# Kernel tuning notes

Measured on AMD Instinct MI355X. Metric: run time of the kernel, lower is better.

## Reference

```python
import jax, jax.numpy as jnp
import numpy as np

GRASPNESS_THRESHOLD = 0.001
M_POINT = 2048
NUM_VIEW = 800
NUM_ANGLE = 12
NUM_DEPTH = 7
B, N, C = 2, 20480, 256
ND, NS = 16384, 512


def generate_grasp_views(n=NUM_VIEW):
    # Fibonacci sphere sampling of unit approach vectors (graspnet convention)
    phi = (np.sqrt(5.0) - 1.0) / 2.0
    i = np.arange(n)
    zi = (2.0 * i + 1.0) / n - 1.0
    r = np.sqrt(np.maximum(1.0 - zi * zi, 0.0))
    xi = r * np.cos(2.0 * np.pi * i * phi)
    yi = r * np.sin(2.0 * np.pi * i * phi)
    return jnp.asarray(np.stack([xi, yi, zi], axis=1), dtype=jnp.float32)  # [n,3], unit norm


def masked_fps(xyz, mask, m):
    # furthest point sampling restricted to mask==True points; xyz [N,3]
    big = jnp.float32(1e10)
    d0 = jnp.where(mask, big, jnp.float32(-1.0))  # invalid never selected
    start = jnp.argmax(mask)  # first valid index (matches compact-then-FPS start at 0)

    def step(carry, _):
        dists, last = carry
        d = jnp.sum((xyz - xyz[last]) ** 2, axis=-1)
        dists = jnp.minimum(dists, jnp.where(mask, d, jnp.float32(-1.0)))
        return (dists, jnp.argmax(dists)), last

    _, idx = jax.lax.scan(step, (d0, start), None, length=m)
    return idx  # [m] int32


def setup_inputs() -> dict:
    key = jax.random.key(0)
    ks = jax.random.split(key, 9)
    return {
        "seed_xyz": jax.random.normal(ks[0], (B, N, 3), jnp.float32),
        "seed_features": jax.random.normal(ks[1], (B, N, C), jnp.float32),
        "graspness_score": jax.random.normal(ks[2], (B, N), jnp.float32),
        "dense_points": jax.random.normal(ks[3], (B, ND, 3), jnp.float32),
        "sparse_points": jax.random.normal(ks[4], (B, NS, 3), jnp.float32),
        "normalized_scores": jax.random.uniform(ks[5], (B, NS), jnp.float32),
        "approach_directions": jax.random.normal(ks[6], (B, NS, 3, 3), jnp.float32),
        "normalized_view_score": jax.random.uniform(ks[7], (B, NS, 3), jnp.float32),
        "normalized_grasp_score": jax.random.uniform(ks[8], (B, NS, 3, NUM_ANGLE, NUM_DEPTH), jnp.float32),
    }


def reference(seed_xyz, seed_features, graspness_score, dense_points, sparse_points,
              normalized_scores, approach_directions, normalized_view_score,
              normalized_grasp_score):
    # ---- stage 1: graspness mask -> masked FPS -> gather xyz/features ----
    graspable = graspness_score > GRASPNESS_THRESHOLD            # [B,N]
    fps_idx = jax.vmap(lambda x, m: masked_fps(x, m, M_POINT))(seed_xyz, graspable)  # [B,M]
    xyz_g = jnp.take_along_axis(seed_xyz, fps_idx[..., None], axis=1)       # [B,M,3]
    feat_g = jnp.take_along_axis(seed_features, fps_idx[..., None], axis=1)  # [B,M,C]

    # ---- stage 2: affordance label via 2-NN of dense points in sparse points ----
    valid = jnp.any(sparse_points != 0.0, axis=-1)               # [B,NS]
    d2 = (jnp.sum(dense_points ** 2, -1)[:, :, None]
          + jnp.sum(sparse_points ** 2, -1)[:, None, :]
          - 2.0 * jnp.einsum('bnd,bmd->bnm', dense_points, sparse_points))  # [B,ND,NS]
    d2 = jnp.where(valid[:, None, :], d2, jnp.float32(1e10))
    _, nn2 = jax.lax.top_k(-d2, 2)                               # [B,ND,2] two nearest
    nn_scores = jax.vmap(lambda s, i: s[i])(normalized_scores, nn2)
    affordance = jnp.mean(nn_scores, axis=-1)                    # [B,ND]

    # ---- stage 3: 1-NN view assignment against 800 template views + scatter ----
    views = generate_grasp_views(NUM_VIEW)                       # [V,3] unit vectors
    # argmin ||a - v||^2 over unit-norm v == argmax a.v
    view_inds = jnp.argmax(jnp.einsum('bnkd,vd->bnkv', approach_directions, views), axis=-1)  # [B,NS,3]
    b_idx = jnp.arange(B)[:, None, None]
    n_idx = jnp.arange(NS)[None, :, None]
    vm = valid.astype(jnp.float32)[:, :, None]                   # zero-out padded sparse rows
    view_scores = jnp.zeros((B, NS, NUM_VIEW), jnp.float32).at[
        b_idx, n_idx, view_inds].set(normalized_view_score * vm)  # [B,NS,V]
    grasp_scores = jnp.zeros((B, NS, NUM_VIEW, NUM_ANGLE, NUM_DEPTH), jnp.float32).at[
        b_idx, n_idx, view_inds].set(normalized_grasp_score * vm[..., None, None])  # [B,NS,V,12,7]
    return xyz_g, feat_g, affordance, view_scores, grasp_scores
```

## Files before the change

kernel.cpp:

```cpp
#include <hip/hip_runtime.h>
#include <math.h>

#define B_   2
#define N_   20480
#define C_   256
#define M_   2048
#define ND_  16384
#define NS_  512
#define NV_  800
#define NAD_ 84

#define OFF_XYZ  0LL
#define OFF_FEAT 12288LL
#define OFF_AFF  1060864LL
#define OFF_VS   1093632LL
#define OFF_GS   1912832LL
#define TOTAL_OUT 70725632LL

#define CAP_ 11264

#define FPS_T 512
#define FPS_P (CAP_ / FPS_T)
#define FPS_W (FPS_T / 64)
#define CPP_  (N_ / FPS_T)

#define NB_FPS 2
#define NB_AFF ((B_ * ND_) / FPS_T)
#define NB_SC  ((B_ * NS_) / FPS_W)
#define GRID_  (NB_FPS + NB_AFF + NB_SC)

union SMem {
    struct {
        float sx[CAP_], sy[CAP_], sz[CAP_];
        alignas(16) unsigned long long s_e[2][FPS_W];
        int s_slot[M_];
        int wsum[FPS_W];
    } fps;
    struct {
        float sx[NS_], sy[NS_], sz[NS_], ss2[NS_], ssc[NS_];
        unsigned char sval[NS_];
    } aff;
    struct { float vx[NV_], vy[NV_], vz[NV_]; } sc;
};

template <int CTRL>
__device__ __forceinline__ unsigned long long dpp_max_u64(unsigned long long k) {
    int olo = __builtin_amdgcn_update_dpp(0, (int)(unsigned)k, CTRL, 0xF, 0xF, true);
    int ohi = __builtin_amdgcn_update_dpp(0, (int)(unsigned)(k >> 32), CTRL, 0xF, 0xF, true);
    unsigned long long ok = ((unsigned long long)(unsigned)ohi << 32) | (unsigned)olo;
    return ok > k ? ok : k;
}

__device__ __forceinline__ unsigned long long wave_argmax_key(unsigned long long k) {
    k = dpp_max_u64<0xB1>(k);
    k = dpp_max_u64<0x4E>(k);
    k = dpp_max_u64<0x141>(k);
    k = dpp_max_u64<0x140>(k);
    k = dpp_max_u64<0x142>(k);
    k = dpp_max_u64<0x143>(k);
    return k;
}

__device__ __forceinline__ unsigned long long group8_max_u64(unsigned long long k) {
    k = dpp_max_u64<0xB1>(k);
    k = dpp_max_u64<0x4E>(k);
    k = dpp_max_u64<0x141>(k);
    return k;
}

__device__ void fps_role(SMem& sm, int b,
                         const float* __restrict__ xyz,
                         const float* __restrict__ gs,
                         int* __restrict__ ic_g, int* __restrict__ fps_idx)
{
    const float* __restrict__ X = xyz + (size_t)b * N_ * 3;
    const float* __restrict__ G = gs + (size_t)b * N_;
    int* __restrict__ IC = ic_g + (size_t)b * CAP_;
    const int t = threadIdx.x, lane = t & 63, wid = t >> 6;

    const int base = t * CPP_;
    int c = 0;
    for (int i = 0; i < CPP_; i++) c += (G[base + i] > 0.001f) ? 1 : 0;
    int inc = c;
#pragma unroll
    for (int o = 1; o < 64; o <<= 1) {
        int v = __shfl_up(inc, o);
        if (lane >= o) inc += v;
    }
    if (lane == 63) sm.fps.wsum[wid] = inc;
    __syncthreads();
    int off = inc - c;
    for (int w = 0; w < wid; w++) off += sm.fps.wsum[w];
    int total = 0;
#pragma unroll
    for (int w = 0; w < FPS_W; w++) total += sm.fps.wsum[w];

    for (int i = 0; i < CPP_; i++) {
        int p = base + i;
        if (G[p] > 0.001f && off < CAP_) {
            sm.fps.sx[off] = X[3 * p];
            sm.fps.sy[off] = X[3 * p + 1];
            sm.fps.sz[off] = X[3 * p + 2];
            IC[off] = p;
            off++;
        }
    }
    const int cv = (total > CAP_) ? CAP_ : total;
    for (int s = cv + t; s < CAP_; s += FPS_T) {
        sm.fps.sx[s] = 0.0f; sm.fps.sy[s] = 0.0f; sm.fps.sz[s] = 0.0f; IC[s] = 0;
    }
    if (t == 0) sm.fps.s_slot[0] = 0;
    __syncthreads();

    float px[FPS_P], py[FPS_P], pz[FPS_P], dd[FPS_P];
#pragma unroll
    for (int i = 0; i < FPS_P; i++) {
        int s = t + FPS_T * i;
        px[i] = sm.fps.sx[s];
        py[i] = sm.fps.sy[s];
        pz[i] = sm.fps.sz[s];
        dd[i] = (s < cv) ? 1e10f : -1.0f;
        asm volatile("" : "+v"(px[i]), "+v"(py[i]), "+v"(pz[i]));
    }
    const int cbase = (lane == 1) ? CAP_ : ((lane == 2) ? 2 * CAP_ : 0);

    float xl = sm.fps.sx[0], yl = sm.fps.sy[0], zl = sm.fps.sz[0];

    for (int it = 1; it < M_; it++) {
        float bv = -2.0f;
        int bli = 0;
#pragma unroll
        for (int i = 0; i < FPS_P; i++) {
            float dx = __fsub_rn(px[i], xl);
            float dy = __fsub_rn(py[i], yl);
            float dz = __fsub_rn(pz[i], zl);
            float d = __fadd_rn(__fadd_rn(__fmul_rn(dx, dx), __fmul_rn(dy, dy)),
                                __fmul_rn(dz, dz));
            float nd = fminf(dd[i], d);
            dd[i] = nd;
            if (nd > bv) { bv = nd; bli = i; }
        }
        unsigned vb = __float_as_uint(bv);
        unsigned mono = (vb & 0x80000000u) ? ~vb : (vb | 0x80000000u);
        int bi = t + FPS_T * bli;
        unsigned long long k = ((unsigned long long)mono << 32)
                             | (unsigned)(0x7FFFFFFF - bi);
        k = wave_argmax_key(k);
        const int par = it & 1;
        if (lane == 63) sm.fps.s_e[par][wid] = k;
        __syncthreads();
        unsigned long long e = sm.fps.s_e[par][lane & 7];
        e = group8_max_u64(e);
        int slot = 0x7FFFFFFF - (int)(unsigned)e;
        if (t == 0) sm.fps.s_slot[it] = slot;
        float cval = sm.fps.sx[cbase + slot];
        int cw = __float_as_int(cval);
        xl = __int_as_float(__builtin_amdgcn_readlane(cw, 0));
        yl = __int_as_float(__builtin_amdgcn_readlane(cw, 1));
        zl = __int_as_float(__builtin_amdgcn_readlane(cw, 2));
    }
    __syncthreads();
    for (int j = t; j < M_; j += FPS_T)
        fps_idx[b * M_ + j] = IC[sm.fps.s_slot[j]];
}

__device__ void aff_role(SMem& sm, int abid,
                         const float* __restrict__ dense,
                         const float* __restrict__ sparse,
                         const float* __restrict__ scores,
                         float* __restrict__ out)
{
    const int t = threadIdx.x;
    const int g = abid * FPS_T + t;
    const int b = g >> 14;
    const int n = g & (ND_ - 1);
    const float* SP = sparse + (size_t)b * NS_ * 3;
    for (int j = t; j < NS_; j += FPS_T) {
        float x = SP[3 * j], y = SP[3 * j + 1], z = SP[3 * j + 2];
        sm.aff.sx[j] = x; sm.aff.sy[j] = y; sm.aff.sz[j] = z;
        sm.aff.ss2[j] = __fadd_rn(__fadd_rn(__fmul_rn(x, x), __fmul_rn(y, y)),
                                  __fmul_rn(z, z));
        sm.aff.sval[j] = (x != 0.0f) || (y != 0.0f) || (z != 0.0f);
        sm.aff.ssc[j] = scores[(size_t)b * NS_ + j];
    }
    __syncthreads();
    const float* D = dense + ((size_t)b * ND_ + n) * 3;
    float x = D[0], y = D[1], z = D[2];
    float ds2 = __fadd_rn(__fadd_rn(__fmul_rn(x, x), __fmul_rn(y, y)),
                          __fmul_rn(z, z));
    float b1 = 1e30f, b2 = 1e30f;
    int i1 = 0, i2 = 0;
    for (int j = 0; j < NS_; j++) {
        float dot = __fadd_rn(__fadd_rn(__fmul_rn(x, sm.aff.sx[j]),
                                        __fmul_rn(y, sm.aff.sy[j])),
                              __fmul_rn(z, sm.aff.sz[j]));
        float d2 = __fsub_rn(__fadd_rn(ds2, sm.aff.ss2[j]), __fmul_rn(2.0f, dot));
        d2 = sm.aff.sval[j] ? d2 : 1e10f;
        if (d2 < b1)      { b2 = b1; i2 = i1; b1 = d2; i1 = j; }
        else if (d2 < b2) { b2 = d2; i2 = j; }
    }
    out[OFF_AFF + (size_t)b * ND_ + n] = (sm.aff.ssc[i1] + sm.aff.ssc[i2]) * 0.5f;
}

__device__ void scatter_role(SMem& sm, int sbid,
                             const float* __restrict__ sparse,
                             const float* __restrict__ appr,
                             const float* __restrict__ nvs,
                             const float* __restrict__ ngs,
                             float* __restrict__ out)
{
    const int t = threadIdx.x;
    for (int i = t; i < NV_; i += FPS_T) {
        const double phi = (sqrt(5.0) - 1.0) * 0.5;
        double zi = (2.0 * (double)i + 1.0) / (double)NV_ - 1.0;
        double r2 = 1.0 - zi * zi;
        if (r2 < 0.0) r2 = 0.0;
        double r = sqrt(r2);
        double ang = ((2.0 * 3.14159265358979311600) * (double)i) * phi;
        sm.sc.vx[i] = (float)(r * cos(ang));
        sm.sc.vy[i] = (float)(r * sin(ang));
        sm.sc.vz[i] = (float)zi;
    }
    const int r0 = sbid * FPS_W;
    {
        float4* vs4 = (float4*)(out + OFF_VS + (size_t)r0 * NV_);
        for (int i = t; i < (FPS_W * NV_) / 4; i += FPS_T)
            vs4[i] = make_float4(0.f, 0.f, 0.f, 0.f);
        float4* gs4 = (float4*)(out + OFF_GS + (size_t)r0 * NV_ * NAD_);
        for (int i = t; i < (FPS_W * NV_ * NAD_) / 4; i += FPS_T)
            gs4[i] = make_float4(0.f, 0.f, 0.f, 0.f);
    }
    __syncthreads();

    const int wid = t >> 6, lane = t & 63;
    const int gw = r0 + wid;
    const int b = gw / NS_, n = gw % NS_;
    const float* SP = sparse + ((size_t)b * NS_ + n) * 3;
    float vm = ((SP[0] != 0.0f) || (SP[1] != 0.0f) || (SP[2] != 0.0f)) ? 1.0f : 0.0f;

    int vind[3];
#pragma unroll
    for (int k = 0; k < 3; k++) {
        const float* A = appr + (((size_t)b * NS_ + n) * 3 + k) * 3;
        float ax = A[0], ay = A[1], az = A[2];
        float bv = -1e30f;
        int bi = 0x7fffffff;
        for (int v = lane; v < NV_; v += 64) {
            float d = __fadd_rn(__fadd_rn(__fmul_rn(ax, sm.sc.vx[v]),
                                          __fmul_rn(ay, sm.sc.vy[v])),
                                __fmul_rn(az, sm.sc.vz[v]));
            if (d > bv) { bv = d; bi = v; }
        }
#pragma unroll
        for (int o = 32; o > 0; o >>= 1) {
            float ov = __shfl_xor(bv, o);
            int   oi = __shfl_xor(bi, o);
            if (ov > bv || (ov == bv && oi < bi)) { bv = ov; bi = oi; }
        }
        vind[k] = bi;
    }
    bool wk0 = (vind[0] != vind[1]) && (vind[0] != vind[2]);
    bool wk1 = (vind[1] != vind[2]);
    bool wk[3] = { wk0, wk1, true };

    size_t row = (size_t)b * NS_ + n;
    if (lane < 3 && wk[lane]) {
        out[OFF_VS + row * NV_ + vind[lane]] = nvs[row * 3 + lane] * vm;
    }
#pragma unroll
    for (int k = 0; k < 3; k++) {
        if (!wk[k]) continue;
        const float* S = ngs + (row * 3 + k) * NAD_;
        float* Dst = out + OFF_GS + (row * NV_ + (size_t)vind[k]) * NAD_;
        for (int j = lane; j < NAD_; j += 64) Dst[j] = S[j] * vm;
    }
}

__global__ __launch_bounds__(FPS_T)
__attribute__((amdgpu_waves_per_eu(2, 2)))
void mega_kernel(
    const float* __restrict__ xyz, const float* __restrict__ gs,
    int* __restrict__ ic_g, int* __restrict__ fps_idx,
    const float* __restrict__ dense, const float* __restrict__ sparse,
    const float* __restrict__ scores, const float* __restrict__ appr,
    const float* __restrict__ nvs, const float* __restrict__ ngs,
    float* __restrict__ out)
{
    __shared__ SMem sm;
    const int bid = blockIdx.x;
    if (bid < NB_FPS) {
        fps_role(sm, bid, xyz, gs, ic_g, fps_idx);
    } else if (bid < NB_FPS + NB_AFF) {
        aff_role(sm, bid - NB_FPS, dense, sparse, scores, out);
    } else {
        scatter_role(sm, bid - NB_FPS - NB_AFF, sparse, appr, nvs, ngs, out);
    }
}

__global__ __launch_bounds__(256) void gather_kernel(
    const float* __restrict__ xyz, const float* __restrict__ feat,
    const int* __restrict__ fps_idx, float* __restrict__ out)
{
    int bm = blockIdx.x;
    int b = bm / M_;
    int idx = fps_idx[bm];
    const float* src = feat + ((size_t)b * N_ + idx) * C_;
    float* dst = out + OFF_FEAT + (size_t)bm * C_;
    dst[threadIdx.x] = src[threadIdx.x];
    if (threadIdx.x < 3)
        out[OFF_XYZ + (size_t)bm * 3 + threadIdx.x] =
            xyz[((size_t)b * N_ + idx) * 3 + threadIdx.x];
}

extern "C" void kernel_launch(void* const* d_in, const int* in_sizes, int n_in,
                              void* d_out, int out_size, void* d_ws, size_t ws_size,
                              hipStream_t stream) {
    const float* seed_xyz      = (const float*)d_in[0];
    const float* seed_features = (const float*)d_in[1];
    const float* graspness     = (const float*)d_in[2];
    const float* dense_points  = (const float*)d_in[3];
    const float* sparse_points = (const float*)d_in[4];
    const float* norm_scores   = (const float*)d_in[5];
    const float* approach      = (const float*)d_in[6];
    const float* nvs           = (const float*)d_in[7];
    const float* ngs           = (const float*)d_in[8];
    float* out = (float*)d_out;

    int* fps_idx = (int*)d_ws;
    int* ic      = (int*)((char*)d_ws + 16384);

    mega_kernel<<<dim3(GRID_), dim3(FPS_T), 0, stream>>>(
        seed_xyz, graspness, ic, fps_idx,
        dense_points, sparse_points, norm_scores,
        approach, nvs, ngs, out);
    gather_kernel<<<dim3(B_ * M_), dim3(256), 0, stream>>>(seed_xyz, seed_features,
                                                           fps_idx, out);
}
```

Before: 2.581 ms.

## Spatially sort FPS candidates into Morton cells and skip waves via bounding-box bounds

Valid points are bucketed into an 8x8x8 Morton-ordered grid with a histogram and scatter, so each thread's contiguous slots hold spatially clustered points. Each wave computes its bounding box, and on every FPS iteration skips the distance update when the lower bound from the new centroid to the box exceeds the wave's current max min-distance, reusing its cached key. Ties are broken by original index to keep the reference argmax order. CAP is reduced slightly. This adds atomics and extra setup passes and depends on exact tie and bound reasoning to stay correct.

```diff
diff --git a/kernel.cpp b/kernel.cpp
--- a/kernel.cpp
+++ b/kernel.cpp
@@ -17,7 +17,7 @@
 #define OFF_GS   1912832LL
 #define TOTAL_OUT 70725632LL
 
-#define CAP_ 11264
+#define CAP_ 10752
 
 #define FPS_T 512
 #define FPS_P (CAP_ / FPS_T)
@@ -35,6 +35,7 @@
         alignas(16) unsigned long long s_e[2][FPS_W];
         int s_slot[M_];
         int wsum[FPS_W];
+        int first_slot;
     } fps;
     struct {
         float sx[NS_], sy[NS_], sz[NS_], ss2[NS_], ssc[NS_];
@@ -50,7 +51,6 @@
     unsigned long long ok = ((unsigned long long)(unsigned)ohi << 32) | (unsigned)olo;
     return ok > k ? ok : k;
 }
-
 __device__ __forceinline__ unsigned long long wave_argmax_key(unsigned long long k) {
     k = dpp_max_u64<0xB1>(k);
     k = dpp_max_u64<0x4E>(k);
@@ -60,12 +60,19 @@
     k = dpp_max_u64<0x143>(k);
     return k;
 }
-
 __device__ __forceinline__ unsigned long long group8_max_u64(unsigned long long k) {
     k = dpp_max_u64<0xB1>(k);
     k = dpp_max_u64<0x4E>(k);
     k = dpp_max_u64<0x141>(k);
     return k;
+}
+
+__device__ __forceinline__ int q8(float v) {
+    int q = (int)floorf(v + 4.0f);
+    return q < 0 ? 0 : (q > 7 ? 7 : q);
+}
+__device__ __forceinline__ int spread3(int v) {
+    return (v & 1) | ((v & 2) << 2) | ((v & 4) << 4);
 }
 
 __device__ void fps_role(SMem& sm, int b,
@@ -77,10 +84,15 @@
     const float* __restrict__ G = gs + (size_t)b * N_;
     int* __restrict__ IC = ic_g + (size_t)b * CAP_;
     const int t = threadIdx.x, lane = t & 63, wid = t >> 6;
-
-    const int base = t * CPP_;
-    int c = 0;
-    for (int i = 0; i < CPP_; i++) c += (G[base + i] > 0.001f) ? 1 : 0;
+    int* hist   = sm.fps.s_slot;
+    int* cursor = sm.fps.s_slot + 512;
+
+    const int base_in = t * CPP_;
+    int c = 0, firstv = 0x7fffffff;
+    for (int i = 0; i < CPP_; i++) {
+        int p = base_in + i;
+        if (G[p] > 0.001f) { c++; if (p < firstv) firstv = p; }
+    }
     int inc = c;
 #pragma unroll
     for (int o = 1; o < 64; o <<= 1) {
@@ -88,70 +100,149 @@
         if (lane >= o) inc += v;
     }
     if (lane == 63) sm.fps.wsum[wid] = inc;
-    __syncthreads();
-    int off = inc - c;
-    for (int w = 0; w < wid; w++) off += sm.fps.wsum[w];
+    if (t == 0) sm.fps.first_slot = 0;
+    hist[t] = 0;
+    __syncthreads();
     int total = 0;
 #pragma unroll
     for (int w = 0; w < FPS_W; w++) total += sm.fps.wsum[w];
+    const int cv = (total > CAP_) ? CAP_ : total;
+    int fv = firstv;
+#pragma unroll
+    for (int o = 32; o > 0; o >>= 1) fv = min(fv, __shfl_xor(fv, o));
+    __syncthreads();
+    if (lane == 0) sm.fps.wsum[wid] = fv;
+    __syncthreads();
+#pragma unroll
+    for (int w = 0; w < FPS_W; w++) fv = min(fv, sm.fps.wsum[w]);
 
     for (int i = 0; i < CPP_; i++) {
-        int p = base + i;
-        if (G[p] > 0.001f && off < CAP_) {
-            sm.fps.sx[off] = X[3 * p];
-            sm.fps.sy[off] = X[3 * p + 1];
-            sm.fps.sz[off] = X[3 * p + 2];
-            IC[off] = p;
-            off++;
+        int p = base_in + i;
+        if (G[p] > 0.001f) {
+            int cell = (spread3(q8(X[3 * p])) << 2)
+                     | (spread3(q8(X[3 * p + 1])) << 1)
+                     | spread3(q8(X[3 * p + 2]));
+            atomicAdd(&hist[cell], 1);
         }
     }
-    const int cv = (total > CAP_) ? CAP_ : total;
+    __syncthreads();
+
+    int hv = hist[t];
+    int hinc = hv;
+#pragma unroll
+    for (int o = 1; o < 64; o <<= 1) {
+        int v = __shfl_up(hinc, o);
+        if (lane >= o) hinc += v;
+    }
+    __syncthreads();
+    if (lane == 63) sm.fps.wsum[wid] = hinc;
+    __syncthreads();
+    int hoff = hinc - hv;
+    for (int w = 0; w < wid; w++) hoff += sm.fps.wsum[w];
+    cursor[t] = hoff;
+    __syncthreads();
+
+    for (int i = 0; i < CPP_; i++) {
+        int p = base_in + i;
+        if (G[p] > 0.001f) {
+            float x = X[3 * p], y = X[3 * p + 1], z = X[3 * p + 2];
+            int cell = (spread3(q8(x)) << 2) | (spread3(q8(y)) << 1)
+                     | spread3(q8(z));
+            int dst = atomicAdd(&cursor[cell], 1);
+            if (dst < CAP_) {
+                sm.fps.sx[dst] = x; sm.fps.sy[dst] = y; sm.fps.sz[dst] = z;
+                IC[dst] = p;
+                if (p == fv) sm.fps.first_slot = dst;
+            }
+        }
+    }
+    __threadfence_block();
+    __syncthreads();
+
+    float tx_ = 0.f, ty_ = 0.f, tz_ = 0.f;
+    if (cv > 0) { tx_ = sm.fps.sx[cv - 1]; ty_ = sm.fps.sy[cv - 1]; tz_ = sm.fps.sz[cv - 1]; }
     for (int s = cv + t; s < CAP_; s += FPS_T) {
-        sm.fps.sx[s] = 0.0f; sm.fps.sy[s] = 0.0f; sm.fps.sz[s] = 0.0f; IC[s] = 0;
-    }
-    if (t == 0) sm.fps.s_slot[0] = 0;
-    __syncthreads();
-
+        sm.fps.sx[s] = tx_; sm.fps.sy[s] = ty_; sm.fps.sz[s] = tz_; IC[s] = 0;
+    }
+    __syncthreads();
+    if (t == 0) sm.fps.s_slot[0] = sm.fps.first_slot;
+    __syncthreads();
+
+    const int pbase = t * FPS_P;
     float px[FPS_P], py[FPS_P], pz[FPS_P], dd[FPS_P];
+    int lkey[FPS_P];
+    float mnx = 1e30f, mxx = -1e30f, mny = 1e30f, mxy = -1e30f,
+          mnz = 1e30f, mxz = -1e30f;
 #pragma unroll
     for (int i = 0; i < FPS_P; i++) {
-        int s = t + FPS_T * i;
-        px[i] = sm.fps.sx[s];
-        py[i] = sm.fps.sy[s];
-        pz[i] = sm.fps.sz[s];
+        int s = pbase + i;
+        px[i] = sm.fps.sx[s]; py[i] = sm.fps.sy[s]; pz[i] = sm.fps.sz[s];
         dd[i] = (s < cv) ? 1e10f : -1.0f;
+        lkey[i] = ((0x7FFF - IC[s]) << 14) | s;
+        mnx = fminf(mnx, px[i]); mxx = fmaxf(mxx, px[i]);
+        mny = fminf(mny, py[i]); mxy = fmaxf(mxy, py[i]);
+        mnz = fminf(mnz, pz[i]); mxz = fmaxf(mxz, pz[i]);
         asm volatile("" : "+v"(px[i]), "+v"(py[i]), "+v"(pz[i]));
     }
+#pragma unroll
+    for (int o = 32; o > 0; o >>= 1) {
+        mnx = fminf(mnx, __shfl_xor(mnx, o)); mxx = fmaxf(mxx, __shfl_xor(mxx, o));
+        mny = fminf(mny, __shfl_xor(mny, o)); mxy = fmaxf(mxy, __shfl_xor(mxy, o));
+        mnz = fminf(mnz, __shfl_xor(mnz, o)); mxz = fmaxf(mxz, __shfl_xor(mxz, o));
+    }
+    const float ctrx = (mnx + mxx) * 0.5f, hfx = (mxx - mnx) * 0.5f * 1.0001f + 1e-6f;
+    const float ctry = (mny + mxy) * 0.5f, hfy = (mxy - mny) * 0.5f * 1.0001f + 1e-6f;
+    const float ctrz = (mnz + mxz) * 0.5f, hfz = (mxz - mnz) * 0.5f * 1.0001f + 1e-6f;
+
     const int cbase = (lane == 1) ? CAP_ : ((lane == 2) ? 2 * CAP_ : 0);
 
-    float xl = sm.fps.sx[0], yl = sm.fps.sy[0], zl = sm.fps.sz[0];
+    const int s0 = sm.fps.s_slot[0];
+    float xl = sm.fps.sx[s0], yl = sm.fps.sy[s0], zl = sm.fps.sz[s0];
+
+    float wub = 1e30f;
+    unsigned cklo = 0, ckhi = 0;
 
     for (int it = 1; it < M_; it++) {
-        float bv = -2.0f;
-        int bli = 0;
-#pragma unroll
-        for (int i = 0; i < FPS_P; i++) {
-            float dx = __fsub_rn(px[i], xl);
-            float dy = __fsub_rn(py[i], yl);
-            float dz = __fsub_rn(pz[i], zl);
-            float d = __fadd_rn(__fadd_rn(__fmul_rn(dx, dx), __fmul_rn(dy, dy)),
-                                __fmul_rn(dz, dz));
-            float nd = fminf(dd[i], d);
-            dd[i] = nd;
-            if (nd > bv) { bv = nd; bli = i; }
+        float ex = fmaxf(fabsf(xl - ctrx) - hfx, 0.f);
+        float ey = fmaxf(fabsf(yl - ctry) - hfy, 0.f);
+        float ez = fmaxf(fabsf(zl - ctrz) - hfz, 0.f);
+        float lb2 = ex * ex + ey * ey + ez * ez;
+        int sk = (lb2 * 0.999f > wub) ? 1 : 0;
+        sk = __builtin_amdgcn_readfirstlane(sk);
+        const int par = it & 1;
+        if (!sk) {
+            float bv = -2.0f;
+            int blk = 0;
+#pragma unroll
+            for (int i = 0; i < FPS_P; i++) {
+                float dx = __fsub_rn(px[i], xl);
+                float dy = __fsub_rn(py[i], yl);
+                float dz = __fsub_rn(pz[i], zl);
+                float d = __fadd_rn(__fadd_rn(__fmul_rn(dx, dx), __fmul_rn(dy, dy)),
+                                    __fmul_rn(dz, dz));
+                float nd = fminf(dd[i], d);
+                dd[i] = nd;
+                bool takeit = (nd > bv) || ((nd == bv) && (lkey[i] > blk));
+                bv  = takeit ? nd : bv;
+                blk = takeit ? lkey[i] : blk;
+            }
+            unsigned vb = __float_as_uint(bv);
+            unsigned mono = vb ^ ((unsigned)((int)vb >> 31) | 0x80000000u);
+            unsigned long long key = ((unsigned long long)mono << 32) | (unsigned)blk;
+            key = wave_argmax_key(key);
+            if (lane == 63) sm.fps.s_e[par][wid] = key;
+            cklo = (unsigned)__builtin_amdgcn_readlane((int)(unsigned)key, 63);
+            ckhi = (unsigned)__builtin_amdgcn_readlane((int)(unsigned)(key >> 32), 63);
+            unsigned vb2 = (ckhi & 0x80000000u) ? (ckhi & 0x7FFFFFFFu) : ~ckhi;
+            wub = __int_as_float((int)vb2);
+        } else {
+            if (lane == 0)
+                sm.fps.s_e[par][wid] = ((unsigned long long)ckhi << 32) | cklo;
         }
-        unsigned vb = __float_as_uint(bv);
-        unsigned mono = (vb & 0x80000000u) ? ~vb : (vb | 0x80000000u);
-        int bi = t + FPS_T * bli;
-        unsigned long long k = ((unsigned long long)mono << 32)
-                             | (unsigned)(0x7FFFFFFF - bi);
-        k = wave_argmax_key(k);
-        const int par = it & 1;
-        if (lane == 63) sm.fps.s_e[par][wid] = k;
         __syncthreads();
         unsigned long long e = sm.fps.s_e[par][lane & 7];
         e = group8_max_u64(e);
-        int slot = 0x7FFFFFFF - (int)(unsigned)e;
+        int slot = (int)(e & 0x3FFFULL);
         if (t == 0) sm.fps.s_slot[it] = slot;
         float cval = sm.fps.sx[cbase + slot];
         int cw = __float_as_int(cval);
```

New measurement: 4.131 ms. 1.6x slower.
